# Optimization experiments

Hardware: AMD Instinct MI355X
Metric: run time of the kernel (lower is better)

Reference implementation:

```python
import jax, jax.numpy as jnp
import numpy as np

BS, H, S, D = 2, 16, 4096, 64
BLOCK = 64
STRIDE_C = 3
NEG = -10000.0


def _global_index(seq_len, block_size, stride_c):
    # static Longformer-style global pattern: first token of each block plus
    # the last `stride_c` tokens of each block
    r = np.arange(seq_len)
    rem = r % block_size
    return np.nonzero((rem == 0) | (rem >= block_size - stride_c))[0]


def setup_inputs() -> dict:
    key = jax.random.key(0)
    k1, k2, k3 = jax.random.split(key, 3)
    q = jax.random.normal(k1, (BS, H, S, D), dtype=jnp.float32)
    k = jax.random.normal(k2, (BS, H, S, D), dtype=jnp.float32)
    v = jax.random.normal(k3, (BS, H, S, D), dtype=jnp.float32)
    mask = jnp.ones((BS, S), dtype=jnp.float32)  # all tokens valid -> pattern is static
    return {"query": q, "key": k, "value": v, "mask": mask}


def reference(query, key, value, mask):
    bs, h, S, d = query.shape
    block = BLOCK
    nb = S // block  # seq_len chosen as multiple of block_size, so pad_len == 0
    g_idx = jnp.asarray(_global_index(S, block, STRIDE_C))  # [G]

    # ---- block-local attention scores ----
    bq = query.reshape(bs, h, nb, block, d)
    bk = key.reshape(bs, h, nb, block, d)
    local = jnp.einsum('bhnxd,bhnyd->bhnxy', bq, bk)  # [bs,h,nb,block,block]
    # additive key-side mask (per key position within each block)
    key_mask = jnp.where(mask == 0.0, NEG, 0.0).reshape(bs, 1, nb, 1, block)
    local = (local + key_mask).reshape(bs, h, S, block)

    # ---- global-token attention scores ----
    gk = key[:, :, g_idx, :]    # [bs,h,G,d]
    gv = value[:, :, g_idx, :]  # [bs,h,G,d]
    gscores = jnp.einsum('bhsd,bhgd->bhsg', query, gk)  # [bs,h,S,G]
    gmask = jnp.where(mask[:, g_idx] == 0.0, NEG, 0.0)[:, None, None, :]
    gscores = gscores + gmask

    # ---- joint softmax over [local block | global tokens] ----
    scores = jnp.concatenate([local, gscores], axis=-1)  # [bs,h,S,block+G]
    probs = jax.nn.softmax(scores.astype(jnp.float32), axis=-1)

    # ---- weighted sums ----
    lp = probs[..., :block].reshape(bs, h, nb, block, block)
    bv = value.reshape(bs, h, nb, block, d)
    lout = jnp.matmul(lp, bv).reshape(bs, h, S, d)
    gout = jnp.einsum('bhsg,bhgd->bhsd', probs[..., block:], gv)
    return lout + gout
```

## Files before the change

kernel.cpp:

```cpp
#include <hip/hip_runtime.h>

#define NEGV -10000.0f

typedef _Float16 f16x8 __attribute__((ext_vector_type(8)));
typedef _Float16 f16x2 __attribute__((ext_vector_type(2)));
typedef float floatx4 __attribute__((ext_vector_type(4)));

__device__ __forceinline__ int src_row(int key, int nblk) {
    if (key < 64) return nblk * 64 + key;
    int g = key - 64;
    int p = g & 3;
    return (g >> 2) * 64 + (p ? (60 + p) : 0);
}

__device__ __forceinline__ f16x8 cvt8(const float4& f0, const float4& f1) {
    f16x8 o;
    o[0] = (_Float16)f0.x; o[1] = (_Float16)f0.y;
    o[2] = (_Float16)f0.z; o[3] = (_Float16)f0.w;
    o[4] = (_Float16)f1.x; o[5] = (_Float16)f1.y;
    o[6] = (_Float16)f1.z; o[7] = (_Float16)f1.w;
    return o;
}

__global__ __launch_bounds__(256, 2)
void sparse_attn_kernel(const float* __restrict__ Q, const float* __restrict__ K,
                        const float* __restrict__ V, const float* __restrict__ M,
                        float* __restrict__ O)
{
    const int x     = blockIdx.x;
    const int bh    = (x & 7) * 4 + ((x >> 3) >> 4);
    const int slice = (x >> 3) & 15;
    const int b     = bh >> 4;
    const int nblk0 = slice * 4;

    const size_t hoff = (size_t)bh * (4096 * 64);
    const float* Qh = Q + hoff;
    const float* Kh = K + hoff;
    const float* Vh = V + hoff;
    float*       Oh = O + hoff;
    const float* Mb = M + (size_t)b * 4096;

    __shared__ _Float16 smem[40960];
    constexpr int GVT = 16384, LKo = 32768, LVT = 36864;

    const int tid  = threadIdx.x;
    const int lane = tid & 63;
    const int wv   = tid >> 6;
    const int m    = lane & 15;
    const int quad = lane >> 4;
    const int cg   = tid & 15;
    const int pg   = tid >> 4;

    auto vt_store_at = [&](int base, int k2, const float4& f0, const float4& f1) {
        int td    = cg >> 2;
        int sw    = td << 4;
        int lbase = base + (k2 * 4 + td) * 512 + (pg >> 2) * 128
                  + (cg & 3) * 32 + 2 * (pg & 3);
        f16x2 pk0; pk0[0] = (_Float16)f0.x; pk0[1] = (_Float16)f1.x;
        *(f16x2*)(&smem[(lbase +  0) ^ sw]) = pk0;
        f16x2 pk1; pk1[0] = (_Float16)f0.y; pk1[1] = (_Float16)f1.y;
        *(f16x2*)(&smem[(lbase +  8) ^ sw]) = pk1;
        f16x2 pk2; pk2[0] = (_Float16)f0.z; pk2[1] = (_Float16)f1.z;
        *(f16x2*)(&smem[(lbase + 16) ^ sw]) = pk2;
        f16x2 pk3; pk3[0] = (_Float16)f0.w; pk3[1] = (_Float16)f1.w;
        *(f16x2*)(&smem[(lbase + 24) ^ sw]) = pk3;
    };
    auto q_load = [&](int nblk, float4* qn) {
        const float* src = Qh + (size_t)(nblk * 64 + wv * 16 + m) * 64 + quad * 8;
        qn[0] = *(const float4*)src;        qn[1] = *(const float4*)(src + 4);
        qn[2] = *(const float4*)(src + 32); qn[3] = *(const float4*)(src + 36);
    };
    auto lk_load = [&](int nblk, float4* kn) {
        #pragma unroll
        for (int s2 = 0; s2 < 2; ++s2) {
            int S    = s2 * 256 + tid;
            int t    = S >> 7;
            int n    = S & 15;
            int col0 = ((S >> 6) & 1) * 32 + ((S & 63) >> 4) * 8;
            int lkey = 32 * (t >> 1) + 8 * (n >> 2) + 4 * (t & 1) + (n & 3);
            const float* src = Kh + (size_t)(nblk * 64 + lkey) * 64 + col0;
            kn[2 * s2]     = *(const float4*)src;
            kn[2 * s2 + 1] = *(const float4*)(src + 4);
        }
    };
    auto lk_write = [&](const float4* kn) {
        #pragma unroll
        for (int s2 = 0; s2 < 2; ++s2) {
            int S = s2 * 256 + tid;
            *(f16x8*)(&smem[LKo + S * 8]) = cvt8(kn[2 * s2], kn[2 * s2 + 1]);
        }
    };
    auto lv_load = [&](int nblk, float4* vn) {
        #pragma unroll
        for (int g = 0; g < 2; ++g) {
            int l0 = 2 * (g * 16 + pg);
            vn[2 * g]     = *(const float4*)(Vh + (size_t)(nblk * 64 + l0) * 64 + cg * 4);
            vn[2 * g + 1] = *(const float4*)(Vh + (size_t)(nblk * 64 + l0 + 1) * 64 + cg * 4);
        }
    };
    auto lv_write = [&](const float4* vn) {
        vt_store_at(LVT, 0, vn[0], vn[1]);
        vt_store_at(LVT, 1, vn[2], vn[3]);
    };

    float mv2[5];
    unsigned long long bbg = 0ull;
    #pragma unroll
    for (int s = 1; s < 5; ++s) {
        float mval = Mb[src_row(s * 64 + lane, 0)];
        bbg |= __ballot(mval == 0.0f);
        mv2[s] = (mval == 0.0f) ? NEGV : 0.0f;
    }

    #pragma unroll
    for (int it = 0; it < 8; ++it) {
        int S    = it * 256 + tid;
        int t    = (S >> 7) + 4;
        int n    = S & 15;
        int col0 = ((S >> 6) & 1) * 32 + ((S & 63) >> 4) * 8;
        int lkey = 32 * (t >> 1) + 8 * (n >> 2) + 4 * (t & 1) + (n & 3);
        const float* src = Kh + (size_t)src_row(lkey, 0) * 64 + col0;
        float4 f0 = *(const float4*)src;
        float4 f1 = *(const float4*)(src + 4);
        *(f16x8*)(&smem[S * 8]) = cvt8(f0, f1);
    }
    #pragma unroll
    for (int it = 2; it < 10; ++it) {
        int l0 = 2 * (it * 16 + pg);
        float4 f0 = *(const float4*)(Vh + (size_t)src_row(l0,     0) * 64 + cg * 4);
        float4 f1 = *(const float4*)(Vh + (size_t)src_row(l0 + 1, 0) * 64 + cg * 4);
        vt_store_at(GVT, it - 2, f0, f1);
    }
    float4 qn[4], kn[4], vn[4];
    q_load(nblk0, qn);
    lk_load(nblk0, kn);
    lv_load(nblk0, vn);
    lk_write(kn);
    lv_write(vn);
    float mloc = Mb[(size_t)nblk0 * 64 + lane];

    __syncthreads();

    #pragma unroll
    for (int i = 0; i < 4; ++i) {
        const int nblk = nblk0 + i;
        f16x8 qf[2] = { cvt8(qn[0], qn[1]), cvt8(qn[2], qn[3]) };
        const float mloc_c = mloc;

        floatx4 acc[20];
        #pragma unroll
        for (int t = 0; t < 20; ++t) {
            acc[t] = floatx4{0.f, 0.f, 0.f, 0.f};
            #pragma unroll
            for (int c = 0; c < 2; ++c) {
                const int slab = (t < 4) ? (LKo + (t * 2 + c) * 512)
                                         : (((t - 4) * 2 + c) * 512);
                f16x8 kf = *(const f16x8*)(&smem[slab + lane * 8]);
                acc[t] = __builtin_amdgcn_mfma_f32_16x16x32_f16(kf, qf[c], acc[t], 0, 0, 0);
            }
        }

        if (i < 3) {
            q_load(nblk + 1, qn);
            lk_load(nblk + 1, kn);
            lv_load(nblk + 1, vn);
            mloc = Mb[(size_t)(nblk + 1) * 64 + lane];
        }

        unsigned long long bb = bbg | __ballot(mloc_c == 0.0f);
        if (bb != 0ull) {
            mv2[0] = (mloc_c == 0.0f) ? NEGV : 0.0f;
            #pragma unroll
            for (int t = 0; t < 20; ++t) {
                int lb = 32 * ((t >> 1) & 1) + 4 * (t & 1) + 8 * quad;
                #pragma unroll
                for (int r = 0; r < 4; ++r)
                    acc[t][r] += __shfl(mv2[t >> 2], lb + r, 64);
            }
        }

        float rmax = -3e38f;
        #pragma unroll
        for (int t = 0; t < 20; ++t)
            #pragma unroll
            for (int r = 0; r < 4; ++r)
                rmax = fmaxf(rmax, acc[t][r]);
        rmax = fmaxf(rmax, __shfl_xor(rmax, 16, 64));
        rmax = fmaxf(rmax, __shfl_xor(rmax, 32, 64));
        float rsum = 0.f;
        #pragma unroll
        for (int t = 0; t < 20; ++t)
            #pragma unroll
            for (int r = 0; r < 4; ++r) {
                float e = __expf(acc[t][r] - rmax);
                acc[t][r] = e;
                rsum += e;
            }
        rsum += __shfl_xor(rsum, 16, 64);
        rsum += __shfl_xor(rsum, 32, 64);
        const float rinv = 1.0f / rsum;

        floatx4 oacc[4] = {};
        #pragma unroll
        for (int k2 = 0; k2 < 10; ++k2) {
            f16x8 p;
            #pragma unroll
            for (int r = 0; r < 4; ++r) {
                p[r]     = (_Float16)(acc[2 * k2][r]     * rinv);
                p[4 + r] = (_Float16)(acc[2 * k2 + 1][r] * rinv);
            }
            #pragma unroll
            for (int t = 0; t < 4; ++t) {
                const int base = (k2 < 2) ? (LVT + (k2 * 4 + t) * 512)
                                          : (GVT + ((k2 - 2) * 4 + t) * 512);
                f16x8 vf = *(const f16x8*)(&smem[base + ((lane * 8) ^ (t << 4))]);
                oacc[t] = __builtin_amdgcn_mfma_f32_16x16x32_f16(p, vf, oacc[t], 0, 0, 0);
            }
        }

        #pragma unroll
        for (int t = 0; t < 4; ++t)
            #pragma unroll
            for (int r = 0; r < 4; ++r)
                Oh[(size_t)(nblk * 64 + wv * 16 + quad * 4 + r) * 64 + t * 16 + m] =
                    oacc[t][r];

        if (i < 3) {
            __syncthreads();
            lk_write(kn);
            lv_write(vn);
            __syncthreads();
        }
    }
}

extern "C" void kernel_launch(void* const* d_in, const int* in_sizes, int n_in,
                              void* d_out, int out_size, void* d_ws, size_t ws_size,
                              hipStream_t stream) {
    const float* q    = (const float*)d_in[0];
    const float* k    = (const float*)d_in[1];
    const float* v    = (const float*)d_in[2];
    const float* mask = (const float*)d_in[3];
    float* out = (float*)d_out;
    (void)in_sizes; (void)n_in; (void)out_size; (void)d_ws; (void)ws_size;
    sparse_attn_kernel<<<512, 256, 0, stream>>>(q, k, v, mask, out);
}
```

Before: 145.3 us.

## Keep local K in registers, double-buffer local V, drop one barrier per block

Local-block K fragments are now loaded by each wave straight from global memory into registers and converted to fp16, rather than staged through shared memory. Local V is double-buffered in shared memory and written before the PV phase, which cuts the per-iteration barriers from two to one. It also adds s_setprio around the MFMA phases and splits the max and sum reductions into four independent chains. The cost is redundant global K loads across the four waves and higher register pressure, which may lower occupancy or cause spills.

```diff
diff --git a/kernel.cpp b/kernel.cpp
--- a/kernel.cpp
+++ b/kernel.cpp
@@ -41,7 +41,7 @@
     const float* Mb = M + (size_t)b * 4096;
 
     __shared__ _Float16 smem[40960];
-    constexpr int GVT = 16384, LKo = 32768, LVT = 36864;
+    constexpr int GVT = 16384, LVT = 32768;
 
     const int tid  = threadIdx.x;
     const int lane = tid & 63;
@@ -70,37 +70,29 @@
         qn[0] = *(const float4*)src;        qn[1] = *(const float4*)(src + 4);
         qn[2] = *(const float4*)(src + 32); qn[3] = *(const float4*)(src + 36);
     };
-    auto lk_load = [&](int nblk, float4* kn) {
-        #pragma unroll
-        for (int s2 = 0; s2 < 2; ++s2) {
-            int S    = s2 * 256 + tid;
-            int t    = S >> 7;
-            int n    = S & 15;
-            int col0 = ((S >> 6) & 1) * 32 + ((S & 63) >> 4) * 8;
-            int lkey = 32 * (t >> 1) + 8 * (n >> 2) + 4 * (t & 1) + (n & 3);
-            const float* src = Kh + (size_t)(nblk * 64 + lkey) * 64 + col0;
-            kn[2 * s2]     = *(const float4*)src;
-            kn[2 * s2 + 1] = *(const float4*)(src + 4);
-        }
-    };
-    auto lk_write = [&](const float4* kn) {
-        #pragma unroll
-        for (int s2 = 0; s2 < 2; ++s2) {
-            int S = s2 * 256 + tid;
-            *(f16x8*)(&smem[LKo + S * 8]) = cvt8(kn[2 * s2], kn[2 * s2 + 1]);
-        }
-    };
-    auto lv_load = [&](int nblk, float4* vn) {
+    auto lk_load = [&](int nblk, float4* kt) {
+        #pragma unroll
+        for (int t = 0; t < 4; ++t) {
+            int lkey = 32 * (t >> 1) + 8 * (m >> 2) + 4 * (t & 1) + (m & 3);
+            const float* row = Kh + (size_t)(nblk * 64 + lkey) * 64 + quad * 8;
+            #pragma unroll
+            for (int c = 0; c < 2; ++c) {
+                kt[(t * 2 + c) * 2]     = *(const float4*)(row + c * 32);
+                kt[(t * 2 + c) * 2 + 1] = *(const float4*)(row + c * 32 + 4);
+            }
+        }
+    };
+    auto lv_load = [&](int nblk, float4* vv) {
         #pragma unroll
         for (int g = 0; g < 2; ++g) {
             int l0 = 2 * (g * 16 + pg);
-            vn[2 * g]     = *(const float4*)(Vh + (size_t)(nblk * 64 + l0) * 64 + cg * 4);
-            vn[2 * g + 1] = *(const float4*)(Vh + (size_t)(nblk * 64 + l0 + 1) * 64 + cg * 4);
-        }
-    };
-    auto lv_write = [&](const float4* vn) {
-        vt_store_at(LVT, 0, vn[0], vn[1]);
-        vt_store_at(LVT, 1, vn[2], vn[3]);
+            vv[2 * g]     = *(const float4*)(Vh + (size_t)(nblk * 64 + l0) * 64 + cg * 4);
+            vv[2 * g + 1] = *(const float4*)(Vh + (size_t)(nblk * 64 + l0 + 1) * 64 + cg * 4);
+        }
+    };
+    auto lv_write = [&](int buf, const float4* vv) {
+        vt_store_at(LVT + buf * 4096, 0, vv[0], vv[1]);
+        vt_store_at(LVT + buf * 4096, 1, vv[2], vv[3]);
     };
 
     float mv2[5];
@@ -131,12 +123,14 @@
         float4 f1 = *(const float4*)(Vh + (size_t)src_row(l0 + 1, 0) * 64 + cg * 4);
         vt_store_at(GVT, it - 2, f0, f1);
     }
-    float4 qn[4], kn[4], vn[4];
+    float4 qn[4], ktmp[16], vn[4];
+    f16x8 lkf[8];
     q_load(nblk0, qn);
-    lk_load(nblk0, kn);
+    lk_load(nblk0, ktmp);
     lv_load(nblk0, vn);
-    lk_write(kn);
-    lv_write(vn);
+    #pragma unroll
+    for (int j = 0; j < 8; ++j) lkf[j] = cvt8(ktmp[2 * j], ktmp[2 * j + 1]);
+    lv_write(0, vn);
     float mloc = Mb[(size_t)nblk0 * 64 + lane];
 
     __syncthreads();
@@ -144,25 +138,27 @@
     #pragma unroll
     for (int i = 0; i < 4; ++i) {
         const int nblk = nblk0 + i;
+        const float mloc_c = mloc;
         f16x8 qf[2] = { cvt8(qn[0], qn[1]), cvt8(qn[2], qn[3]) };
-        const float mloc_c = mloc;
 
         floatx4 acc[20];
+        __builtin_amdgcn_s_setprio(1);
         #pragma unroll
         for (int t = 0; t < 20; ++t) {
             acc[t] = floatx4{0.f, 0.f, 0.f, 0.f};
             #pragma unroll
             for (int c = 0; c < 2; ++c) {
-                const int slab = (t < 4) ? (LKo + (t * 2 + c) * 512)
-                                         : (((t - 4) * 2 + c) * 512);
-                f16x8 kf = *(const f16x8*)(&smem[slab + lane * 8]);
+                f16x8 kf;
+                if (t < 4) kf = lkf[t * 2 + c];
+                else       kf = *(const f16x8*)(&smem[((t - 4) * 2 + c) * 512 + lane * 8]);
                 acc[t] = __builtin_amdgcn_mfma_f32_16x16x32_f16(kf, qf[c], acc[t], 0, 0, 0);
             }
         }
+        __builtin_amdgcn_s_setprio(0);
 
         if (i < 3) {
             q_load(nblk + 1, qn);
-            lk_load(nblk + 1, kn);
+            lk_load(nblk + 1, ktmp);
             lv_load(nblk + 1, vn);
             mloc = Mb[(size_t)(nblk + 1) * 64 + lane];
         }
@@ -179,28 +175,38 @@
             }
         }
 
-        float rmax = -3e38f;
+        float rmax4[4] = {-3e38f, -3e38f, -3e38f, -3e38f};
         #pragma unroll
         for (int t = 0; t < 20; ++t)
             #pragma unroll
             for (int r = 0; r < 4; ++r)
-                rmax = fmaxf(rmax, acc[t][r]);
+                rmax4[r] = fmaxf(rmax4[r], acc[t][r]);
+        float rmax = fmaxf(fmaxf(rmax4[0], rmax4[1]), fmaxf(rmax4[2], rmax4[3]));
         rmax = fmaxf(rmax, __shfl_xor(rmax, 16, 64));
         rmax = fmaxf(rmax, __shfl_xor(rmax, 32, 64));
-        float rsum = 0.f;
+        float rsum4[4] = {0.f, 0.f, 0.f, 0.f};
         #pragma unroll
         for (int t = 0; t < 20; ++t)
             #pragma unroll
             for (int r = 0; r < 4; ++r) {
                 float e = __expf(acc[t][r] - rmax);
                 acc[t][r] = e;
-                rsum += e;
-            }
+                rsum4[r] += e;
+            }
+        float rsum = (rsum4[0] + rsum4[1]) + (rsum4[2] + rsum4[3]);
         rsum += __shfl_xor(rsum, 16, 64);
         rsum += __shfl_xor(rsum, 32, 64);
         const float rinv = 1.0f / rsum;
 
+        if (i < 3) {
+            lv_write((i + 1) & 1, vn);
+            #pragma unroll
+            for (int j = 0; j < 8; ++j) lkf[j] = cvt8(ktmp[2 * j], ktmp[2 * j + 1]);
+        }
+
+        const int lvbase = LVT + (i & 1) * 4096;
         floatx4 oacc[4] = {};
+        __builtin_amdgcn_s_setprio(1);
         #pragma unroll
         for (int k2 = 0; k2 < 10; ++k2) {
             f16x8 p;
@@ -211,12 +217,13 @@
             }
             #pragma unroll
             for (int t = 0; t < 4; ++t) {
-                const int base = (k2 < 2) ? (LVT + (k2 * 4 + t) * 512)
+                const int base = (k2 < 2) ? (lvbase + (k2 * 4 + t) * 512)
                                           : (GVT + ((k2 - 2) * 4 + t) * 512);
                 f16x8 vf = *(const f16x8*)(&smem[base + ((lane * 8) ^ (t << 4))]);
                 oacc[t] = __builtin_amdgcn_mfma_f32_16x16x32_f16(p, vf, oacc[t], 0, 0, 0);
             }
         }
+        __builtin_amdgcn_s_setprio(0);
 
         #pragma unroll
         for (int t = 0; t < 4; ++t)
@@ -225,12 +232,7 @@
                 Oh[(size_t)(nblk * 64 + wv * 16 + quad * 4 + r) * 64 + t * 16 + m] =
                     oacc[t][r];
 
-        if (i < 3) {
-            __syncthreads();
-            lk_write(kn);
-            lv_write(vn);
-            __syncthreads();
-        }
+        if (i < 3) __syncthreads();
     }
 }
 
```

Result: slower. 150.7 us (+3.7%).
